# Kernel tuning notes

Hardware: AMD Instinct MI355X
Metric: run time of the kernel (lower is better)

## Reference

```python
import jax, jax.numpy as jnp
import numpy as np

N = 32768   # nodes
E = 32768   # edges
ND, ED, GD = 12, 5, 11
H = 64
T = 4
STEPS = 3


def setup_inputs() -> dict:
    key = jax.random.key(0)
    ks = jax.random.split(key, 24)
    s = 0.05
    p = lambda k, sh: (jax.random.normal(k, sh) * s).astype(jnp.float32)
    return dict(
        x=jax.random.normal(ks[0], (N, ND), jnp.float32),
        edge_index=jax.random.randint(ks[1], (2, E), 0, N, jnp.int64),
        edge_attr=jax.random.uniform(ks[2], (E, ED), jnp.float32),
        u=jax.random.normal(ks[3], (1, GD), jnp.float32),
        Wp=p(ks[4], (H, ND + GD)), bp=p(ks[5], (H,)),
        We1=p(ks[6], (H, ED)), be1=p(ks[7], (H,)),
        We2=p(ks[8], (H * H, H)), be2=p(ks[9], (H * H,)),
        root=p(ks[10], (H, H)), conv_b=p(ks[11], (H,)),
        Wih=p(ks[12], (3 * H, H)), bih=p(ks[13], (3 * H,)),
        Whh=p(ks[14], (3 * H, H)), bhh=p(ks[15], (3 * H,)),
        Wd1=p(ks[16], (H, 2 * H + ED)), bd1=p(ks[17], (H,)),
        Wd2=p(ks[18], (H // 2, H)), bd2=p(ks[19], (H // 2,)),
        Wd3=p(ks[20], (T, H // 2)), bd3=p(ks[21], (T,)),
    )


def _forward(x, edge_index, edge_attr, u,
             Wp, bp, We1, be1, We2, be2, root, conv_b,
             Wih, bih, Whh, bhh, Wd1, bd1, Wd2, bd2, Wd3, bd3):
    n = x.shape[0]
    e = edge_attr.shape[0]
    src, dst = edge_index[0], edge_index[1]

    # input projection with broadcast global features (batch=None path)
    u_node = jnp.broadcast_to(u, (n, u.shape[-1]))
    h = jnp.tanh(jnp.concatenate([x, u_node], axis=-1) @ Wp.T + bp)

    # edge MLP -> per-edge (H,H) weight matrices; edge_attr is loop-invariant
    ew = jax.nn.relu(edge_attr @ We1.T + be1) @ We2.T + be2   # (E, H*H)
    ew = ew.reshape(e, H, H)                                   # (E, H, H)

    # mean-aggregation denominators (clamped to 1 like scatter-mean)
    counts = jnp.clip(jax.ops.segment_sum(jnp.ones((e,), h.dtype), dst, num_segments=n), 1.0)

    for _ in range(STEPS):
        # NNConv: gather src features, per-edge matmul, scatter-mean into dst
        msg = jnp.einsum('eh,eho->eo', h[src], ew)             # (E, H)
        agg = jax.ops.segment_sum(msg, dst, num_segments=n) / counts[:, None]
        m = jax.nn.relu(agg + h @ root + conv_b)               # dropout off (eval)
        # GRUCell (torch gate order: r, z, n)
        gi = m @ Wih.T + bih
        gh = h @ Whh.T + bhh
        r = jax.nn.sigmoid(gi[:, :H] + gh[:, :H])
        z = jax.nn.sigmoid(gi[:, H:2 * H] + gh[:, H:2 * H])
        ng = jnp.tanh(gi[:, 2 * H:] + r * gh[:, 2 * H:])
        h = (1.0 - z) * ng + z * h

    # per-edge decoder
    e_in = jnp.concatenate([h[src], h[dst], edge_attr], axis=-1)
    d = jax.nn.relu(e_in @ Wd1.T + bd1)
    d = jax.nn.relu(d @ Wd2.T + bd2)
    return d @ Wd3.T + bd3                                     # (E, T)


def reference(x, edge_index, edge_attr, u,
              Wp, bp, We1, be1, We2, be2, root, conv_b,
              Wih, bih, Whh, bhh, Wd1, bd1, Wd2, bd2, Wd3, bd3):
    return _forward(x, edge_index, edge_attr, u,
                    Wp, bp, We1, be1, We2, be2, root, conv_b,
                    Wih, bih, Whh, bhh, Wd1, bd1, Wd2, bd2, Wd3, bd3)
```

## Files before the change

kernel.cpp:

```cpp
#include <hip/hip_runtime.h>
#include <hip/hip_bf16.h>
#include <stdint.h>


#define N_NODES 32768
#define N_EDGES 32768
#define STEPS 3

typedef __attribute__((ext_vector_type(8))) short short8;
typedef __attribute__((ext_vector_type(4))) float float4v;

__device__ __forceinline__ float bf2f(unsigned short u) {
    union { unsigned int i; float f; } v; v.i = ((unsigned int)u) << 16; return v.f;
}
__device__ __forceinline__ unsigned short f2bf(float f) {
    union { float f; unsigned int i; } v; v.f = f;
    unsigned int x = v.i;
    return (unsigned short)((x + 0x7fffu + ((x >> 16) & 1u)) >> 16);
}
__device__ __forceinline__ unsigned int fbits(float f) {
    union { float f; unsigned int i; } v; v.f = f; return v.i;
}

__device__ __forceinline__ short8 packA(float hv, const float* hf) {
    union { short8 v; unsigned int u[4]; } r;
#pragma unroll
    for (int p = 0; p < 4; p++) {
        unsigned int p0 = fbits(hv * hf[2 * p]) + 0x8000u;
        unsigned int p1 = fbits(hv * hf[2 * p + 1]) + 0x8000u;
        r.u[p] = __builtin_amdgcn_perm(p1, p0, 0x07060302u);
    }
    return r.v;
}

__device__ __forceinline__ void gload_lds16(const void* g, void* l) {
    __builtin_amdgcn_global_load_lds(
        (__attribute__((address_space(1))) void*)g,
        (__attribute__((address_space(3))) void*)l, 16, 0, 0);
}

__global__ __launch_bounds__(256) void k_setup(
    const float* __restrict__ root, const float* __restrict__ Wih,
    const float* __restrict__ Whh,
    const float* __restrict__ We2, const float* __restrict__ be2,
    const float* __restrict__ Wd1, const float* __restrict__ bd1,
    const float* __restrict__ Wd2,
    const float* __restrict__ x, const float* __restrict__ u,
    const float* __restrict__ Wp, const float* __restrict__ bp,
    const float* __restrict__ ea, const float* __restrict__ We1,
    const float* __restrict__ be1,
    unsigned short* __restrict__ rootTf, unsigned short* __restrict__ wcombf,
    unsigned short* __restrict__ w2tf,
    unsigned short* __restrict__ wd1f, unsigned short* __restrict__ wd2f,
    unsigned short* __restrict__ hb,
    unsigned short* __restrict__ hid, float* __restrict__ aggcnt)
{
    int b = blockIdx.x, tid = threadIdx.x;
    if (b < 144) {
        int i = b * 256 + tid;
        if (i < 4096) {
            int j = i & 7, lane = (i >> 3) & 63, g = i >> 9;
            int kb = g >> 2, nf = g & 3;
            int o = nf * 16 + (lane & 15);
            int k = kb * 32 + (lane >> 4) * 8 + j;
            rootTf[i] = f2bf(root[k * 64 + o]);
        } else if (i < 4096 + 32768) {
            int t = i - 4096;
            int j = t & 7, lane = (t >> 3) & 63, g = t >> 9;
            int kb = g >> 4, nf = g & 15;
            int cp = nf * 16 + (lane & 15);
            int k = kb * 32 + (lane >> 4) * 8 + j;
            float v;
            if (cp < 128)      v = (k < 64) ? Wih[cp * 64 + k] : Whh[cp * 64 + (k - 64)];
            else if (cp < 192) v = (k < 64) ? Wih[cp * 64 + k] : 0.f;
            else               v = (k < 64) ? 0.f : Whh[(cp - 64) * 64 + (k - 64)];
            wcombf[t] = f2bf(v);
        }
    } else if (b < 1184) {
        int t = (b - 144) * 256 + tid;
        if (t < 65 * 4096) {
            int kk = t >> 12, r = t & 4095;
            int j = r & 7, lane = (r >> 3) & 63, g = r >> 9;
            int half = g >> 2, nf = g & 3;
            int o = nf * 16 + (lane & 15);
            int hh = half * 32 + (lane >> 4) * 8 + j;
            float v = (kk < 64) ? We2[((size_t)(hh * 64 + o)) * 64 + kk]
                                : be2[(size_t)hh * 64 + o];
            w2tf[t] = f2bf(v);
        }
    } else if (b < 1232) {
        int i = (b - 1184) * 256 + tid;
        if (i < 10240) {
            int j = i & 7, lane = (i >> 3) & 63, g = i >> 9;
            int kb = g >> 2, nf = g & 3;
            int o = nf * 16 + (lane & 15);
            int k = kb * 32 + (lane >> 4) * 8 + j;
            float v = (k < 133) ? Wd1[(size_t)o * 133 + k] : (k == 133 ? bd1[o] : 0.f);
            wd1f[i] = f2bf(v);
        } else if (i < 10240 + 2048) {
            int t = i - 10240;
            int j = t & 7, lane = (t >> 3) & 63, g = t >> 9;
            int kb = g >> 1, nf = g & 1;
            int o = nf * 16 + (lane & 15);
            int k = kb * 32 + (lane >> 4) * 8 + j;
            wd2f[t] = f2bf(Wd2[(size_t)o * 64 + k]);
        }
    } else if (b < 9424) {
        int idx = (b - 1232) * 256 + tid;
        int n = idx >> 6, j = idx & 63;
        const float* wr = Wp + j * 23;
        const float* xr = x + (size_t)n * 12;
        float s = bp[j];
#pragma unroll
        for (int i = 0; i < 12; i++) s += xr[i] * wr[i];
#pragma unroll
        for (int i = 0; i < 11; i++) s += u[i] * wr[12 + i];
        hb[idx] = f2bf(tanhf(s));
    } else if (b < 17616) {
        int idx = (b - 9424) * 256 + tid;
        int e = idx >> 6, j = idx & 63;
        float s = be1[j];
#pragma unroll
        for (int i = 0; i < 5; i++) s += ea[(size_t)e * 5 + i] * We1[j * 5 + i];
        hid[idx] = f2bf(s > 0.f ? s : 0.f);
    } else {
        int idx = (b - 17616) * 1024 + tid * 4;
        if (idx < 2129920) {
            float4v z = {0.f, 0.f, 0.f, 0.f};
            *(float4v*)(aggcnt + idx) = z;
        }
    }
}

__global__ __launch_bounds__(256) void k_counts(
    const int* __restrict__ ei, float* __restrict__ counts)
{
    int i = blockIdx.x * 256 + threadIdx.x;
    if (i < N_EDGES) atomicAdd(&counts[ei[N_EDGES + i]], 1.0f);
}

__global__ __launch_bounds__(512, 4) void k_msg_fused(
    const unsigned short* __restrict__ hid,
    const unsigned short* __restrict__ hb,
    const unsigned short* __restrict__ w2tf,
    const int* __restrict__ ei,
    float* __restrict__ agg)
{
    __shared__ unsigned short buf[2][2][8192];
    int tid = threadIdx.x, wave = tid >> 6, lane = tid & 63;
    int l15 = lane & 15, quad = lane >> 4;
    int mf = wave & 3, kh = wave >> 2;
    int ebase = blockIdx.x * 64 + mf * 16;
    int e_a = ebase + l15;
    int src = ei[e_a];

    union { short8 v[4]; unsigned short u[32]; } hrow;
#pragma unroll
    for (int i = 0; i < 4; i++)
        hrow.v[i] = *(const short8*)(hid + (size_t)e_a * 64 + kh * 32 + i * 8);

    float hf0[8], hf1[8];
    {
        short8 h0 = *(const short8*)(hb + (size_t)src * 64 + quad * 8);
        short8 h1 = *(const short8*)(hb + (size_t)src * 64 + 32 + quad * 8);
#pragma unroll
        for (int j = 0; j < 8; j++) {
            hf0[j] = bf2f((unsigned short)h0[j]);
            hf1[j] = bf2f((unsigned short)h1[j]);
        }
    }

    int kk0 = kh ? 32 : 0;
    auto stage = [&](int pair, int db) {
        const unsigned short* g = w2tf + (size_t)(kk0 + 2 * pair) * 4096;
#pragma unroll
        for (int c = 0; c < 4; c++) {
            int chunk = mf * 4 + c;
            gload_lds16(g + (size_t)chunk * 512 + lane * 8, &buf[kh][db][chunk * 512]);
        }
    };

    stage(0, 0);

    float4v acc[4] = {};
    int cur = 0;
#pragma unroll
    for (int i = 0; i <= 16; i++) {
        __syncthreads();
        if ((kh == 0 && i + 1 < 16) || (kh == 1 && i + 1 <= 16))
            stage(i + 1, cur ^ 1);
        int nkk = (kh == 0) ? (i < 16 ? 2 : 0) : (i < 16 ? 2 : 1);
        for (int s = 0; s < nkk; s++) {
            float hv = (kh == 1 && i == 16) ? 1.0f : bf2f(hrow.u[2 * i + s]);
            short8 a0 = packA(hv, hf0);
            short8 a1 = packA(hv, hf1);
            const unsigned short* bp = &buf[kh][cur][s * 4096];
#pragma unroll
            for (int nf = 0; nf < 4; nf++) {
                short8 b0 = *(const short8*)(bp + (0 * 4 + nf) * 512 + lane * 8);
                acc[nf] = __builtin_amdgcn_mfma_f32_16x16x32_bf16(a0, b0, acc[nf], 0, 0, 0);
            }
#pragma unroll
            for (int nf = 0; nf < 4; nf++) {
                short8 b1 = *(const short8*)(bp + (1 * 4 + nf) * 512 + lane * 8);
                acc[nf] = __builtin_amdgcn_mfma_f32_16x16x32_bf16(a1, b1, acc[nf], 0, 0, 0);
            }
        }
        cur ^= 1;
    }

    __syncthreads();
    float* mg = (float*)&buf[0][0][0];
    if (kh == 1) {
#pragma unroll
        for (int nf = 0; nf < 4; nf++)
#pragma unroll
            for (int r = 0; r < 4; r++)
                mg[mf * 1024 + lane * 16 + nf * 4 + r] = acc[nf][r];
    }
    __syncthreads();
    if (kh == 0) {
        int dsts[4];
#pragma unroll
        for (int r = 0; r < 4; r++) dsts[r] = ei[N_EDGES + ebase + quad * 4 + r];
#pragma unroll
        for (int nf = 0; nf < 4; nf++)
#pragma unroll
            for (int r = 0; r < 4; r++)
                atomicAdd(agg + (size_t)dsts[r] * 64 + nf * 16 + l15,
                          acc[nf][r] + mg[mf * 1024 + lane * 16 + nf * 4 + r]);
    }
}

__global__ __launch_bounds__(256) void k_node(
    const unsigned short* __restrict__ hb_in,
    const unsigned short* __restrict__ rootTf,
    const unsigned short* __restrict__ wcombf,
    float* __restrict__ agg, const float* __restrict__ counts,
    const float* __restrict__ conv_b,
    const float* __restrict__ bih, const float* __restrict__ bhh,
    unsigned short* __restrict__ hb_out)
{
    __shared__ unsigned short m_lds[64 * 72];
    int tid = threadIdx.x, w = tid >> 6, lane = tid & 63;
    int l15 = lane & 15, quad = lane >> 4;
    int node0 = blockIdx.x * 64;
    int row0 = w * 16;

    float4v acc1[4] = {};
    {
        short8 a1[2];
#pragma unroll
        for (int kb = 0; kb < 2; kb++)
            a1[kb] = *(const short8*)(hb_in + (size_t)(node0 + row0 + l15) * 64 + kb * 32 + quad * 8);
#pragma unroll
        for (int kb = 0; kb < 2; kb++)
#pragma unroll
            for (int nf = 0; nf < 4; nf++) {
                short8 b = *(const short8*)(rootTf + (size_t)((kb * 4 + nf) * 64 + lane) * 8);
                acc1[nf] = __builtin_amdgcn_mfma_f32_16x16x32_bf16(a1[kb], b, acc1[nf], 0, 0, 0);
            }
    }
#pragma unroll
    for (int rr = 0; rr < 4; rr++) {
        int nl = row0 + quad * 4 + rr;
        float cnt = counts[node0 + nl]; if (cnt < 1.f) cnt = 1.f;
        float rcp = 1.f / cnt;
#pragma unroll
        for (int nf = 0; nf < 4; nf++) {
            int c = nf * 16 + l15;
            float* ap = agg + (size_t)(node0 + nl) * 64 + c;
            float av = *ap;
            *ap = 0.f;
            float mv = av * rcp + acc1[nf][rr] + conv_b[c];
            m_lds[nl * 72 + c] = f2bf(mv > 0.f ? mv : 0.f);
        }
    }
    __syncthreads();

    float4v acc2[16] = {};
#pragma unroll
    for (int kb = 0; kb < 4; kb++) {
        short8 a2;
        if (kb < 2)
            a2 = *(const short8*)(m_lds + (row0 + l15) * 72 + kb * 32 + quad * 8);
        else
            a2 = *(const short8*)(hb_in + (size_t)(node0 + row0 + l15) * 64 + (kb - 2) * 32 + quad * 8);
#pragma unroll
        for (int nf = 0; nf < 16; nf++) {
            short8 b = *(const short8*)(wcombf + (size_t)((kb * 16 + nf) * 64 + lane) * 8);
            acc2[nf] = __builtin_amdgcn_mfma_f32_16x16x32_bf16(a2, b, acc2[nf], 0, 0, 0);
        }
    }

#pragma unroll
    for (int nf0 = 0; nf0 < 4; nf0++) {
        int c = nf0 * 16 + l15;
        float br = bih[c] + bhh[c];
        float bz = bih[64 + c] + bhh[64 + c];
        float bni = bih[128 + c], bnh = bhh[128 + c];
#pragma unroll
        for (int rr = 0; rr < 4; rr++) {
            int node = node0 + row0 + quad * 4 + rr;
            float gr = 1.f / (1.f + __expf(-(acc2[nf0][rr] + br)));
            float gz = 1.f / (1.f + __expf(-(acc2[nf0 + 4][rr] + bz)));
            float ng = tanhf(acc2[nf0 + 8][rr] + bni + gr * (acc2[nf0 + 12][rr] + bnh));
            float ho = bf2f(hb_in[(size_t)node * 64 + c]);
            float hn = (1.f - gz) * ng + gz * ho;
            hb_out[(size_t)node * 64 + c] = f2bf(hn);
        }
    }
}

__global__ __launch_bounds__(256) void k_decoder(
    const unsigned short* __restrict__ hb, const int* __restrict__ ei,
    const float* __restrict__ ea,
    const unsigned short* __restrict__ wd1f, const unsigned short* __restrict__ wd2f,
    const float* __restrict__ bd2,
    const float* __restrict__ Wd3, const float* __restrict__ bd3,
    float* __restrict__ out)
{
    __shared__ unsigned short d1f[4][1024];
    __shared__ float d2s[4][16 * 33];
    int tid = threadIdx.x, w = tid >> 6, lane = tid & 63;
    int l15 = lane & 15, quad = lane >> 4;
    int ebase = blockIdx.x * 64 + w * 16;
    int e = ebase + l15;
    int src = ei[e], dst = ei[N_EDGES + e];

    short8 a[5];
#pragma unroll
    for (int kb = 0; kb < 2; kb++) {
        a[kb]     = *(const short8*)(hb + (size_t)src * 64 + kb * 32 + quad * 8);
        a[2 + kb] = *(const short8*)(hb + (size_t)dst * 64 + kb * 32 + quad * 8);
    }
    {
        union { short8 v; unsigned short u[8]; } tea;
#pragma unroll
        for (int j = 0; j < 8; j++) {
            float vv = 0.f;
            if (quad == 0) vv = (j < 5) ? ea[(size_t)e * 5 + j] : (j == 5 ? 1.f : 0.f);
            tea.u[j] = f2bf(vv);
        }
        a[4] = tea.v;
    }

    float4v acc1[4] = {};
#pragma unroll
    for (int kb = 0; kb < 5; kb++)
#pragma unroll
        for (int nf = 0; nf < 4; nf++) {
            short8 b = *(const short8*)(wd1f + (size_t)((kb * 4 + nf) * 64 + lane) * 8);
            acc1[nf] = __builtin_amdgcn_mfma_f32_16x16x32_bf16(a[kb], b, acc1[nf], 0, 0, 0);
        }
#pragma unroll
    for (int nf = 0; nf < 4; nf++) {
        int kbp = nf >> 1;
        int lanep_hi = ((nf & 1) * 2 + (l15 >> 3)) * 16;
        int jp = l15 & 7;
#pragma unroll
        for (int r = 0; r < 4; r++) {
            float v = acc1[nf][r];
            d1f[w][kbp * 512 + (lanep_hi + quad * 4 + r) * 8 + jp] = f2bf(v > 0.f ? v : 0.f);
        }
    }
    float4v acc2[2] = {};
#pragma unroll
    for (int kb = 0; kb < 2; kb++) {
        short8 a2 = *(const short8*)(&d1f[w][kb * 512 + lane * 8]);
#pragma unroll
        for (int nf = 0; nf < 2; nf++) {
            short8 b = *(const short8*)(wd2f + (size_t)((kb * 2 + nf) * 64 + lane) * 8);
            acc2[nf] = __builtin_amdgcn_mfma_f32_16x16x32_bf16(a2, b, acc2[nf], 0, 0, 0);
        }
    }
#pragma unroll
    for (int nf = 0; nf < 2; nf++) {
        int c = nf * 16 + l15;
        float bias = bd2[c];
#pragma unroll
        for (int r = 0; r < 4; r++) {
            float v = acc2[nf][r] + bias;
            d2s[w][(quad * 4 + r) * 33 + c] = v > 0.f ? v : 0.f;
        }
    }
    {
        int e_l = lane >> 2, t = lane & 3;
        float s = bd3[t];
        const float* w3 = Wd3 + t * 32;
        const float* dr = &d2s[w][e_l * 33];
#pragma unroll
        for (int k = 0; k < 32; k++) s += w3[k] * dr[k];
        out[(size_t)(ebase + e_l) * 4 + t] = s;
    }
}

extern "C" void kernel_launch(void* const* d_in, const int* in_sizes, int n_in,
                              void* d_out, int out_size, void* d_ws, size_t ws_size,
                              hipStream_t stream)
{
    const float* x      = (const float*)d_in[0];
    const int*   ei     = (const int*)d_in[1];
    const float* ea     = (const float*)d_in[2];
    const float* u      = (const float*)d_in[3];
    const float* Wp     = (const float*)d_in[4];
    const float* bp     = (const float*)d_in[5];
    const float* We1    = (const float*)d_in[6];
    const float* be1    = (const float*)d_in[7];
    const float* We2    = (const float*)d_in[8];
    const float* be2    = (const float*)d_in[9];
    const float* root   = (const float*)d_in[10];
    const float* conv_b = (const float*)d_in[11];
    const float* Wih    = (const float*)d_in[12];
    const float* bih    = (const float*)d_in[13];
    const float* Whh    = (const float*)d_in[14];
    const float* bhh    = (const float*)d_in[15];
    const float* Wd1    = (const float*)d_in[16];
    const float* bd1    = (const float*)d_in[17];
    const float* Wd2    = (const float*)d_in[18];
    const float* bd2    = (const float*)d_in[19];
    const float* Wd3    = (const float*)d_in[20];
    const float* bd3    = (const float*)d_in[21];
    float* out = (float*)d_out;

    char* ws = (char*)d_ws;
    size_t off = 0;
    auto take = [&](size_t bytes) -> char* {
        char* p = ws + off; off = (off + bytes + 255) & ~(size_t)255; return p;
    };
    unsigned short* hb     = (unsigned short*)take((size_t)N_NODES * 64 * 2);
    unsigned short* hid    = (unsigned short*)take((size_t)N_EDGES * 64 * 2);
    float*          aggcnt = (float*)take((size_t)(N_NODES * 64 + N_NODES) * 4);
    float*          agg    = aggcnt;
    float*          cnts   = aggcnt + (size_t)N_NODES * 64;
    unsigned short* w2tf   = (unsigned short*)take((size_t)66 * 4096 * 2);
    unsigned short* rootTf = (unsigned short*)take((size_t)4096 * 2);
    unsigned short* wcombf = (unsigned short*)take((size_t)32768 * 2);
    unsigned short* wd1f   = (unsigned short*)take((size_t)10240 * 2);
    unsigned short* wd2f   = (unsigned short*)take((size_t)2048 * 2);
    (void)ws_size;

    k_setup<<<19696, 256, 0, stream>>>(root, Wih, Whh, We2, be2, Wd1, bd1, Wd2,
                                       x, u, Wp, bp, ea, We1, be1,
                                       rootTf, wcombf, w2tf, wd1f, wd2f,
                                       hb, hid, aggcnt);
    k_counts<<<128, 256, 0, stream>>>(ei, cnts);

    for (int s = 0; s < STEPS; s++) {
        k_msg_fused<<<N_EDGES / 64, 512, 0, stream>>>(hid, hb, w2tf, ei, agg);
        k_node<<<N_NODES / 64, 256, 0, stream>>>(hb, rootTf, wcombf, agg, cnts,
                                                 conv_b, bih, bhh, hb);
    }
    k_decoder<<<N_EDGES / 64, 256, 0, stream>>>(hb, ei, ea, wd1f, wd2f, bd2,
                                                Wd3, bd3, out);
}
```

Before: 271.8 us.

## Restructure edge message kernel to reuse h-gather fragments across per-k weight slices

Rewrites the per-edge message computation so each wave handles 16 (or 17, including the bias slice) k-slices of the edge-MLP weight for all 64 edges. The gathered h[src] fragments are loaded once as MFMA A operands, and the scalar hidden activation is applied as an fp32 post-multiply rather than being baked into a repacked A operand per k. Hidden activations are stored transposed (feature-major) so each block can stage them into LDS. Per-wave partial sums are reduced through LDS before the atomics. This removes the per-step packA conversion work and block-wide barriers, at the cost of more accumulator registers, more fp32 FMAs, and a 72KB LDS footprint that limits occupancy.

```diff
diff --git a/kernel.cpp b/kernel.cpp
--- a/kernel.cpp
+++ b/kernel.cpp
@@ -17,20 +17,6 @@
     union { float f; unsigned int i; } v; v.f = f;
     unsigned int x = v.i;
     return (unsigned short)((x + 0x7fffu + ((x >> 16) & 1u)) >> 16);
-}
-__device__ __forceinline__ unsigned int fbits(float f) {
-    union { float f; unsigned int i; } v; v.f = f; return v.i;
-}
-
-__device__ __forceinline__ short8 packA(float hv, const float* hf) {
-    union { short8 v; unsigned int u[4]; } r;
-#pragma unroll
-    for (int p = 0; p < 4; p++) {
-        unsigned int p0 = fbits(hv * hf[2 * p]) + 0x8000u;
-        unsigned int p1 = fbits(hv * hf[2 * p + 1]) + 0x8000u;
-        r.u[p] = __builtin_amdgcn_perm(p1, p0, 0x07060302u);
-    }
-    return r.v;
 }
 
 __device__ __forceinline__ void gload_lds16(const void* g, void* l) {
@@ -53,7 +39,7 @@
     unsigned short* __restrict__ w2tf,
     unsigned short* __restrict__ wd1f, unsigned short* __restrict__ wd2f,
     unsigned short* __restrict__ hb,
-    unsigned short* __restrict__ hid, float* __restrict__ aggcnt)
+    unsigned short* __restrict__ hidT, float* __restrict__ aggcnt)
 {
     int b = blockIdx.x, tid = threadIdx.x;
     if (b < 144) {
@@ -118,11 +104,12 @@
         hb[idx] = f2bf(tanhf(s));
     } else if (b < 17616) {
         int idx = (b - 9424) * 256 + tid;
-        int e = idx >> 6, j = idx & 63;
+        int el = idx & 63, j = (idx >> 6) & 63, eb = idx >> 12;
+        int e = eb * 64 + el;
         float s = be1[j];
 #pragma unroll
         for (int i = 0; i < 5; i++) s += ea[(size_t)e * 5 + i] * We1[j * 5 + i];
-        hid[idx] = f2bf(s > 0.f ? s : 0.f);
+        hidT[(size_t)j * N_EDGES + e] = f2bf(s > 0.f ? s : 0.f);
     } else {
         int idx = (b - 17616) * 1024 + tid * 4;
         if (idx < 2129920) {
@@ -139,96 +126,119 @@
     if (i < N_EDGES) atomicAdd(&counts[ei[N_EDGES + i]], 1.0f);
 }
 
-__global__ __launch_bounds__(512, 4) void k_msg_fused(
-    const unsigned short* __restrict__ hid,
+__global__ __launch_bounds__(256, 2) void k_msg_fused(
+    const unsigned short* __restrict__ hidT,
     const unsigned short* __restrict__ hb,
     const unsigned short* __restrict__ w2tf,
     const int* __restrict__ ei,
     float* __restrict__ agg)
 {
-    __shared__ unsigned short buf[2][2][8192];
-    int tid = threadIdx.x, wave = tid >> 6, lane = tid & 63;
+    __shared__ __attribute__((aligned(16))) unsigned char smem[73728];
+    unsigned short* stg = (unsigned short*)smem;
+    unsigned short* hvl = (unsigned short*)(smem + 65536);
+    float* red = (float*)smem;
+
+    int tid = threadIdx.x, w = tid >> 6, lane = tid & 63;
     int l15 = lane & 15, quad = lane >> 4;
-    int mf = wave & 3, kh = wave >> 2;
-    int ebase = blockIdx.x * 64 + mf * 16;
-    int e_a = ebase + l15;
-    int src = ei[e_a];
-
-    union { short8 v[4]; unsigned short u[32]; } hrow;
-#pragma unroll
-    for (int i = 0; i < 4; i++)
-        hrow.v[i] = *(const short8*)(hid + (size_t)e_a * 64 + kh * 32 + i * 8);
-
-    float hf0[8], hf1[8];
+    int ebase = blockIdx.x * 64;
+    int n = 16 + (w == 3 ? 1 : 0);
+
     {
-        short8 h0 = *(const short8*)(hb + (size_t)src * 64 + quad * 8);
-        short8 h1 = *(const short8*)(hb + (size_t)src * 64 + 32 + quad * 8);
-#pragma unroll
-        for (int j = 0; j < 8; j++) {
-            hf0[j] = bf2f((unsigned short)h0[j]);
-            hf1[j] = bf2f((unsigned short)h1[j]);
-        }
-    }
-
-    int kk0 = kh ? 32 : 0;
-    auto stage = [&](int pair, int db) {
-        const unsigned short* g = w2tf + (size_t)(kk0 + 2 * pair) * 4096;
-#pragma unroll
-        for (int c = 0; c < 4; c++) {
-            int chunk = mf * 4 + c;
-            gload_lds16(g + (size_t)chunk * 512 + lane * 8, &buf[kh][db][chunk * 512]);
-        }
+        const unsigned short* hp = hidT + (size_t)(w * 16) * N_EDGES + ebase + lane;
+        unsigned short* dp = hvl + (w * 16) * 64 + lane;
+#pragma unroll
+        for (int r = 0; r < 16; r++)
+            dp[r * 64] = hp[(size_t)r * N_EDGES];
+    }
+    short8 afr[4][2];
+#pragma unroll
+    for (int t = 0; t < 4; t++) {
+        int src = ei[ebase + t * 16 + l15];
+#pragma unroll
+        for (int hh = 0; hh < 2; hh++)
+            afr[t][hh] = *(const short8*)(hb + (size_t)src * 64 + hh * 32 + quad * 8);
+    }
+
+    unsigned short* wbuf = stg + w * (2 * 4096);
+    auto stage = [&](int r, int db) {
+        const unsigned short* g = w2tf + (size_t)(w * 16 + r) * 4096;
+        unsigned short* d = wbuf + db * 4096;
+#pragma unroll
+        for (int c = 0; c < 8; c++)
+            gload_lds16(g + c * 512 + lane * 8, d + c * 512);
     };
 
     stage(0, 0);
-
-    float4v acc[4] = {};
-    int cur = 0;
-#pragma unroll
-    for (int i = 0; i <= 16; i++) {
-        __syncthreads();
-        if ((kh == 0 && i + 1 < 16) || (kh == 1 && i + 1 <= 16))
-            stage(i + 1, cur ^ 1);
-        int nkk = (kh == 0) ? (i < 16 ? 2 : 0) : (i < 16 ? 2 : 1);
-        for (int s = 0; s < nkk; s++) {
-            float hv = (kh == 1 && i == 16) ? 1.0f : bf2f(hrow.u[2 * i + s]);
-            short8 a0 = packA(hv, hf0);
-            short8 a1 = packA(hv, hf1);
-            const unsigned short* bp = &buf[kh][cur][s * 4096];
+    stage(1, 1);
+
+    float4v acc[4][4] = {};
+    for (int r = 0; r < n; r++) {
+        int db = r & 1;
+        if (r < n - 1) { asm volatile("s_waitcnt vmcnt(8)" ::: "memory"); }
+        else           { asm volatile("s_waitcnt vmcnt(0)" ::: "memory"); }
+
+        short8 bfr[2][4];
+        const unsigned short* bb = wbuf + db * 4096;
+#pragma unroll
+        for (int hh = 0; hh < 2; hh++)
+#pragma unroll
+            for (int nf = 0; nf < 4; nf++)
+                bfr[hh][nf] = *(const short8*)(bb + (hh * 4 + nf) * 512 + lane * 8);
+
+        bool bias = (r == 16);
+        unsigned long long hu[4] = {0ull, 0ull, 0ull, 0ull};
+        if (!bias) {
+#pragma unroll
+            for (int t = 0; t < 4; t++)
+                hu[t] = *(const unsigned long long*)(hvl + (w * 16 + r) * 64 + t * 16 + quad * 4);
+        }
+
+        asm volatile("s_waitcnt lgkmcnt(0)" ::: "memory");
+        if (r + 2 < n) stage(r + 2, db);
+
+#pragma unroll
+        for (int t = 0; t < 4; t++) {
+            float4v T[4];
 #pragma unroll
             for (int nf = 0; nf < 4; nf++) {
-                short8 b0 = *(const short8*)(bp + (0 * 4 + nf) * 512 + lane * 8);
-                acc[nf] = __builtin_amdgcn_mfma_f32_16x16x32_bf16(a0, b0, acc[nf], 0, 0, 0);
+                float4v z = {0.f, 0.f, 0.f, 0.f};
+                T[nf] = __builtin_amdgcn_mfma_f32_16x16x32_bf16(afr[t][0], bfr[0][nf], z, 0, 0, 0);
             }
 #pragma unroll
-            for (int nf = 0; nf < 4; nf++) {
-                short8 b1 = *(const short8*)(bp + (1 * 4 + nf) * 512 + lane * 8);
-                acc[nf] = __builtin_amdgcn_mfma_f32_16x16x32_bf16(a1, b1, acc[nf], 0, 0, 0);
+            for (int nf = 0; nf < 4; nf++)
+                T[nf] = __builtin_amdgcn_mfma_f32_16x16x32_bf16(afr[t][1], bfr[1][nf], T[nf], 0, 0, 0);
+#pragma unroll
+            for (int rr = 0; rr < 4; rr++) {
+                float hvv = bias ? 1.0f : bf2f((unsigned short)(hu[t] >> (16 * rr)));
+#pragma unroll
+                for (int nf = 0; nf < 4; nf++)
+                    acc[t][nf][rr] += hvv * T[nf][rr];
             }
         }
-        cur ^= 1;
     }
 
     __syncthreads();
-    float* mg = (float*)&buf[0][0][0];
-    if (kh == 1) {
+    float* rp = red + w * 4224;
+#pragma unroll
+    for (int t = 0; t < 4; t++)
 #pragma unroll
         for (int nf = 0; nf < 4; nf++)
 #pragma unroll
-            for (int r = 0; r < 4; r++)
-                mg[mf * 1024 + lane * 16 + nf * 4 + r] = acc[nf][r];
-    }
+            for (int rr = 0; rr < 4; rr++)
+                rp[(t * 16 + quad * 4 + rr) * 66 + nf * 16 + l15] = acc[t][nf][rr];
     __syncthreads();
-    if (kh == 0) {
-        int dsts[4];
-#pragma unroll
-        for (int r = 0; r < 4; r++) dsts[r] = ei[N_EDGES + ebase + quad * 4 + r];
-#pragma unroll
-        for (int nf = 0; nf < 4; nf++)
-#pragma unroll
-            for (int r = 0; r < 4; r++)
-                atomicAdd(agg + (size_t)dsts[r] * 64 + nf * 16 + l15,
-                          acc[nf][r] + mg[mf * 1024 + lane * 16 + nf * 4 + r]);
+    {
+        int row = tid >> 2, c0 = (tid & 3) * 16;
+        int dst = ei[N_EDGES + ebase + row];
+        float* ap = agg + (size_t)dst * 64 + c0;
+#pragma unroll
+        for (int k = 0; k < 16; k++) {
+            float s = 0.f;
+#pragma unroll
+            for (int ww = 0; ww < 4; ww++)
+                s += red[ww * 4224 + row * 66 + c0 + k];
+            atomicAdd(ap + k, s);
+        }
     }
 }
 
@@ -429,7 +439,7 @@
         char* p = ws + off; off = (off + bytes + 255) & ~(size_t)255; return p;
     };
     unsigned short* hb     = (unsigned short*)take((size_t)N_NODES * 64 * 2);
-    unsigned short* hid    = (unsigned short*)take((size_t)N_EDGES * 64 * 2);
+    unsigned short* hidT   = (unsigned short*)take((size_t)N_EDGES * 64 * 2);
     float*          aggcnt = (float*)take((size_t)(N_NODES * 64 + N_NODES) * 4);
     float*          agg    = aggcnt;
     float*          cnts   = aggcnt + (size_t)N_NODES * 64;
@@ -443,11 +453,11 @@
     k_setup<<<19696, 256, 0, stream>>>(root, Wih, Whh, We2, be2, Wd1, bd1, Wd2,
                                        x, u, Wp, bp, ea, We1, be1,
                                        rootTf, wcombf, w2tf, wd1f, wd2f,
-                                       hb, hid, aggcnt);
+                                       hb, hidT, aggcnt);
     k_counts<<<128, 256, 0, stream>>>(ei, cnts);
 
     for (int s = 0; s < STEPS; s++) {
-        k_msg_fused<<<N_EDGES / 64, 512, 0, stream>>>(hid, hb, w2tf, ei, agg);
+        k_msg_fused<<<N_EDGES / 64, 256, 0, stream>>>(hidT, hb, w2tf, ei, agg);
         k_node<<<N_NODES / 64, 256, 0, stream>>>(hb, rootTf, wcombf, agg, cnts,
                                                  conv_b, bih, bhh, hb);
     }
```

Result: slower. 590.0 us (+117.1%).
